# Performance work log

Measured on AMD Instinct MI355X. Metric: run time of the kernel, lower is better.

Reference implementation:

```python
import jax, jax.numpy as jnp
import numpy as np

B, W, C_BLK, N_EMBD, N_HEADS = 512, 128, 24, 32, 2


def setup_inputs() -> dict:
    key = jax.random.key(0)
    k1, k2, k3, k4 = jax.random.split(key, 4)
    x = jax.random.normal(k1, (B, W, C_BLK, N_EMBD), dtype=jnp.float32)
    x_end_idx = jax.random.randint(k2, (B, W), 0, C_BLK, dtype=jnp.int32)
    # nn.Linear(n_embd, 3*n_embd, bias=False): store transposed so y = x @ w
    w_attn = jax.random.normal(k3, (N_EMBD, 3 * N_EMBD), dtype=jnp.float32) * (1.0 / np.sqrt(N_EMBD))
    w_proj = jax.random.normal(k4, (N_EMBD, N_EMBD), dtype=jnp.float32) * (1.0 / np.sqrt(N_EMBD))
    return {"x": x, "x_end_idx": x_end_idx, "w_attn": w_attn, "w_proj": w_proj}


def reference(x, x_end_idx, w_attn, w_proj):
    # x: [B, W, c, C]; causal self-attention over the char axis c, per (batch, word).
    Bd, Wd, c, C = x.shape
    H = N_HEADS
    D = C // H
    qkv = x @ w_attn                               # [B, W, c, 3C]
    q, k, v = jnp.split(qkv, 3, axis=-1)
    # [B, W, H, c, D]
    q = q.reshape(Bd, Wd, c, H, D).transpose(0, 1, 3, 2, 4)
    k = k.reshape(Bd, Wd, c, H, D).transpose(0, 1, 3, 2, 4)
    v = v.reshape(Bd, Wd, c, H, D).transpose(0, 1, 3, 2, 4)
    scale = 1.0 / jnp.sqrt(jnp.asarray(D, dtype=x.dtype))
    scores = jnp.einsum('bwhqd,bwhkd->bwhqk', q, k) * scale   # [B, W, H, c, c]
    causal = jnp.tril(jnp.ones((c, c), dtype=bool))
    scores = jnp.where(causal, scores, jnp.asarray(-jnp.inf, dtype=scores.dtype))
    att = jax.nn.softmax(scores, axis=-1)
    out = jnp.einsum('bwhqk,bwhkd->bwhqd', att, v)            # [B, W, H, c, D]
    out = out.transpose(0, 1, 3, 2, 4).reshape(Bd, Wd, c, C)
    out = out @ w_proj                                        # c_proj (dropout in eval mode = identity)
    out = x + out                                             # residual
    # Vectorized last-token gather: pick out[b, w, x_end_idx[b, w], :]
    idx = x_end_idx[:, :, None, None].astype(jnp.int32)       # [B, W, 1, 1]
    samples = jnp.take_along_axis(out, jnp.broadcast_to(idx, (Bd, Wd, 1, C)), axis=2)
    return samples.squeeze(2)                                 # [B, W, C]
```

## Files before the change

### kernel.cpp

```cpp
#include <hip/hip_runtime.h>


#define CB      24
#define CC      32
#define DD      16
#define THREEC  96
#define NBW     (512 * 128)
#define WPB     4
#define XSS     34

struct __align__(16) WaveSmem {
    float xs[CB][XSS];
    float rks[2][CC];
    float es[CB][2];
    float ys[CC][2];
};

__device__ __forceinline__ void wave_fence() {
    __asm__ volatile("s_waitcnt lgkmcnt(0)" ::: "memory");
}

__global__ void prep_kernel(const float* __restrict__ w_attn,
                            const float* __restrict__ w_proj,
                            float* __restrict__ ws)
{
    const int t = blockIdx.x * 256 + threadIdx.x;
    if (t < 2048) {
        const int h = t >> 10, rem = t & 1023, cp = rem >> 5, c = rem & 31;
        float a = 0.f;
        #pragma unroll
        for (int d = 0; d < DD; ++d)
            a = fmaf(w_attn[cp * THREEC + 16 * h + d],
                     w_attn[c * THREEC + CC + 16 * h + d], a);
        ws[t] = a * 0.25f;
    } else {
        const int u = t - 2048;
        const int h = u >> 10, rem = u & 1023, c = rem >> 5, i = rem & 31;
        float a = 0.f;
        #pragma unroll
        for (int d = 0; d < DD; ++d)
            a = fmaf(w_attn[c * THREEC + 2 * CC + 16 * h + d],
                     w_proj[(16 * h + d) * CC + i], a);
        ws[t] = a;
    }
}

__global__ __launch_bounds__(256, 4) void char_attn_kernel(
    const float* __restrict__ x,
    const int*   __restrict__ xend,
    const float* __restrict__ ws,
    float*       __restrict__ out)
{
    __shared__ WaveSmem sm[WPB];

    const int tid  = threadIdx.x;
    const int lane = tid & 63;
    const int wave = tid >> 6;
    WaveSmem& S = sm[wave];

    const int i32  = lane & 31;
    const int half = lane >> 5;
    const int bid  = blockIdx.x * WPB + wave;

    const float* Mw = ws;
    const float* Nw = ws + 2048;

    float Mreg[CC];
    #pragma unroll
    for (int cp = 0; cp < CC; ++cp)
        Mreg[cp] = Mw[(half * CC + cp) * CC + i32];
    float Nreg[2][DD];
    #pragma unroll
    for (int h = 0; h < 2; ++h)
        #pragma unroll
        for (int k = 0; k < DD; ++k)
            Nreg[h][k] = Nw[(h * CC + half * DD + k) * CC + i32];

    const int qidx = xend[bid];
    const int L    = qidx + 1;
    const float* xb = x + (size_t)bid * (CB * CC);

    {
        const float2* xb2 = (const float2*)xb;
        const int n2 = L * (CC / 2);
        for (int t = lane; t < n2; t += 64) {
            float2 v = xb2[t];
            const int r = t >> 4, c = (t & 15) * 2;
            *(float2*)&S.xs[r][c] = v;
        }
    }
    wave_fence();

    {
        float a0 = 0.f, a1 = 0.f;
        #pragma unroll
        for (int cp = 0; cp < CC; cp += 2) {
            float2 xv = *(const float2*)&S.xs[qidx][cp];
            a0 = fmaf(xv.x, Mreg[cp],     a0);
            a1 = fmaf(xv.y, Mreg[cp + 1], a1);
        }
        S.rks[half][i32] = a0 + a1;
    }
    wave_fence();

    {
        float s0 = 0.f, s1 = 0.f;
        if (i32 <= qidx) {
            const int cb = half * DD;
            #pragma unroll
            for (int t = 0; t < DD; t += 2) {
                float2 xv = *(const float2*)&S.xs[i32][cb + t];
                s0 = fmaf(xv.x, S.rks[0][cb + t],     s0);
                s0 = fmaf(xv.y, S.rks[0][cb + t + 1], s0);
                s1 = fmaf(xv.x, S.rks[1][cb + t],     s1);
                s1 = fmaf(xv.y, S.rks[1][cb + t + 1], s1);
            }
        }
        s0 += __shfl_xor(s0, 32);
        s1 += __shfl_xor(s1, 32);
        const float e0 = (i32 <= qidx) ? __expf(s0) : 0.f;
        const float e1 = (i32 <= qidx) ? __expf(s1) : 0.f;
        if (half == 0 && i32 < CB)
            *(float2*)&S.es[i32][0] = make_float2(e0, e1);
    }
    wave_fence();

    {
        float y0 = 0.f, y1 = 0.f, ps0 = 0.f, ps1 = 0.f;
        #pragma unroll
        for (int jj = 0; jj < 12; ++jj) {
            const int j  = half * 12 + jj;
            const int jr = (j <= qidx) ? j : qidx;
            float2 ev = *(const float2*)&S.es[j][0];
            float  xv = S.xs[jr][i32];
            y0 = fmaf(ev.x, xv, y0);  ps0 += ev.x;
            y1 = fmaf(ev.y, xv, y1);  ps1 += ev.y;
        }
        y0  += __shfl_xor(y0, 32);
        y1  += __shfl_xor(y1, 32);
        ps0 += __shfl_xor(ps0, 32);
        ps1 += __shfl_xor(ps1, 32);
        if (half == 0)
            *(float2*)&S.ys[i32][0] = make_float2(y0 / ps0, y1 / ps1);
    }
    wave_fence();

    {
        float a0 = 0.f, a1 = 0.f;
        #pragma unroll
        for (int k = 0; k < DD; ++k) {
            const int c = half * DD + k;
            float2 yv = *(const float2*)&S.ys[c][0];
            a0 = fmaf(yv.x, Nreg[0][k], a0);
            a1 = fmaf(yv.y, Nreg[1][k], a1);
        }
        float a = a0 + a1;
        a += __shfl_xor(a, 32);
        if (half == 0)
            out[(size_t)bid * CC + i32] = a + S.xs[qidx][i32];
    }
}

extern "C" void kernel_launch(void* const* d_in, const int* in_sizes, int n_in,
                              void* d_out, int out_size, void* d_ws, size_t ws_size,
                              hipStream_t stream) {
    const float* x      = (const float*)d_in[0];
    const int*   xend   = (const int*)d_in[1];
    const float* w_attn = (const float*)d_in[2];
    const float* w_proj = (const float*)d_in[3];
    float* out = (float*)d_out;
    float* ws  = (float*)d_ws;

    prep_kernel<<<dim3(16), dim3(256), 0, stream>>>(w_attn, w_proj, ws);
    char_attn_kernel<<<dim3(NBW / WPB), dim3(WPB * 64), 0, stream>>>(
        x, xend, ws, out);
}
```

Baseline: 304.2 us.

## Process eight words per wave to amortize weight register loads

Each wave now loops over eight (batch, word) problems instead of one. The per-thread M and N weight registers are loaded once and reused across all eight, and the grid shrinks by the same factor. The shared-memory layouts change (row stride padded to 36, transposed rki and ys) so the inner products can use float4 LDS reads. The risk is less parallelism to hide global load latency, because the x loads inside the serial loop are not prefetched; grid size drops to 2048 blocks.

New measurement: 305.3 us. Within noise of the previous version (+0.4%).

```diff
diff --git a/kernel.cpp b/kernel.cpp
--- a/kernel.cpp
+++ b/kernel.cpp
@@ -7,13 +7,14 @@
 #define THREEC  96
 #define NBW     (512 * 128)
 #define WPB     4
-#define XSS     34
+#define PPW     8
+#define XSS     36
 
 struct __align__(16) WaveSmem {
     float xs[CB][XSS];
-    float rks[2][CC];
+    float rki[CC][2];
     float es[CB][2];
-    float ys[CC][2];
+    float ys[2][CC];
 };
 
 __device__ __forceinline__ void wave_fence() {
@@ -60,7 +61,8 @@
 
     const int i32  = lane & 31;
     const int half = lane >> 5;
-    const int bid  = blockIdx.x * WPB + wave;
+    const int wid  = blockIdx.x * WPB + wave;
+    const int pbase = wid * PPW;
 
     const float* Mw = ws;
     const float* Nw = ws + 2048;
@@ -76,88 +78,111 @@
         for (int k = 0; k < DD; ++k)
             Nreg[h][k] = Nw[(h * CC + half * DD + k) * CC + i32];
 
-    const int qidx = xend[bid];
-    const int L    = qidx + 1;
-    const float* xb = x + (size_t)bid * (CB * CC);
-
-    {
-        const float2* xb2 = (const float2*)xb;
-        const int n2 = L * (CC / 2);
-        for (int t = lane; t < n2; t += 64) {
-            float2 v = xb2[t];
-            const int r = t >> 4, c = (t & 15) * 2;
-            *(float2*)&S.xs[r][c] = v;
-        }
-    }
-    wave_fence();
-
-    {
-        float a0 = 0.f, a1 = 0.f;
-        #pragma unroll
-        for (int cp = 0; cp < CC; cp += 2) {
-            float2 xv = *(const float2*)&S.xs[qidx][cp];
-            a0 = fmaf(xv.x, Mreg[cp],     a0);
-            a1 = fmaf(xv.y, Mreg[cp + 1], a1);
-        }
-        S.rks[half][i32] = a0 + a1;
-    }
-    wave_fence();
-
-    {
-        float s0 = 0.f, s1 = 0.f;
-        if (i32 <= qidx) {
-            const int cb = half * DD;
+    #pragma unroll 1
+    for (int pi = 0; pi < PPW; ++pi) {
+        const int bid  = pbase + pi;
+        const int qidx = xend[bid];
+        const int L    = qidx + 1;
+        const float* xb = x + (size_t)bid * (CB * CC);
+
+        {
+            const float2* xb2 = (const float2*)xb;
+            const int n2 = L * (CC / 2);
+            for (int t = lane; t < n2; t += 64) {
+                float2 v = xb2[t];
+                const int r = t >> 4, c = (t & 15) * 2;
+                *(float2*)&S.xs[r][c] = v;
+            }
+        }
+        wave_fence();
+
+        {
+            const float4* xr = (const float4*)&S.xs[qidx][0];
+            float a0 = 0.f, a1 = 0.f;
             #pragma unroll
-            for (int t = 0; t < DD; t += 2) {
-                float2 xv = *(const float2*)&S.xs[i32][cb + t];
-                s0 = fmaf(xv.x, S.rks[0][cb + t],     s0);
-                s0 = fmaf(xv.y, S.rks[0][cb + t + 1], s0);
-                s1 = fmaf(xv.x, S.rks[1][cb + t],     s1);
-                s1 = fmaf(xv.y, S.rks[1][cb + t + 1], s1);
-            }
-        }
-        s0 += __shfl_xor(s0, 32);
-        s1 += __shfl_xor(s1, 32);
-        const float e0 = (i32 <= qidx) ? __expf(s0) : 0.f;
-        const float e1 = (i32 <= qidx) ? __expf(s1) : 0.f;
-        if (half == 0 && i32 < CB)
-            *(float2*)&S.es[i32][0] = make_float2(e0, e1);
-    }
-    wave_fence();
-
-    {
-        float y0 = 0.f, y1 = 0.f, ps0 = 0.f, ps1 = 0.f;
-        #pragma unroll
-        for (int jj = 0; jj < 12; ++jj) {
-            const int j  = half * 12 + jj;
-            const int jr = (j <= qidx) ? j : qidx;
-            float2 ev = *(const float2*)&S.es[j][0];
-            float  xv = S.xs[jr][i32];
-            y0 = fmaf(ev.x, xv, y0);  ps0 += ev.x;
-            y1 = fmaf(ev.y, xv, y1);  ps1 += ev.y;
-        }
-        y0  += __shfl_xor(y0, 32);
-        y1  += __shfl_xor(y1, 32);
-        ps0 += __shfl_xor(ps0, 32);
-        ps1 += __shfl_xor(ps1, 32);
-        if (half == 0)
-            *(float2*)&S.ys[i32][0] = make_float2(y0 / ps0, y1 / ps1);
-    }
-    wave_fence();
-
-    {
-        float a0 = 0.f, a1 = 0.f;
-        #pragma unroll
-        for (int k = 0; k < DD; ++k) {
-            const int c = half * DD + k;
-            float2 yv = *(const float2*)&S.ys[c][0];
-            a0 = fmaf(yv.x, Nreg[0][k], a0);
-            a1 = fmaf(yv.y, Nreg[1][k], a1);
-        }
-        float a = a0 + a1;
-        a += __shfl_xor(a, 32);
-        if (half == 0)
-            out[(size_t)bid * CC + i32] = a + S.xs[qidx][i32];
+            for (int t = 0; t < 8; ++t) {
+                float4 xv = xr[t];
+                a0 = fmaf(xv.x, Mreg[4 * t + 0], a0);
+                a1 = fmaf(xv.y, Mreg[4 * t + 1], a1);
+                a0 = fmaf(xv.z, Mreg[4 * t + 2], a0);
+                a1 = fmaf(xv.w, Mreg[4 * t + 3], a1);
+            }
+            S.rki[i32][half] = a0 + a1;
+        }
+        wave_fence();
+
+        {
+            float s0 = 0.f, s1 = 0.f;
+            if (i32 <= qidx) {
+                const int cb = half * DD;
+                const float4* xr = (const float4*)&S.xs[i32][cb];
+                const float4* rp = (const float4*)&S.rki[cb][0];
+                #pragma unroll
+                for (int t = 0; t < 4; ++t) {
+                    float4 xv = xr[t];
+                    float4 r01 = rp[2 * t];
+                    float4 r23 = rp[2 * t + 1];
+                    s0 = fmaf(xv.x, r01.x, s0);  s1 = fmaf(xv.x, r01.y, s1);
+                    s0 = fmaf(xv.y, r01.z, s0);  s1 = fmaf(xv.y, r01.w, s1);
+                    s0 = fmaf(xv.z, r23.x, s0);  s1 = fmaf(xv.z, r23.y, s1);
+                    s0 = fmaf(xv.w, r23.z, s0);  s1 = fmaf(xv.w, r23.w, s1);
+                }
+            }
+            s0 += __shfl_xor(s0, 32);
+            s1 += __shfl_xor(s1, 32);
+            const float e0 = (i32 <= qidx) ? __expf(s0) : 0.f;
+            const float e1 = (i32 <= qidx) ? __expf(s1) : 0.f;
+            if (half == 0 && i32 < CB)
+                *(float2*)&S.es[i32][0] = make_float2(e0, e1);
+        }
+        wave_fence();
+
+        {
+            float y0 = 0.f, y1 = 0.f, p0 = 0.f, p1 = 0.f;
+            #pragma unroll
+            for (int k = 0; k < 6; ++k) {
+                const int j0 = half * 12 + 2 * k;
+                float4 eq = *(const float4*)&S.es[j0][0];
+                const int r0 = (j0     <= qidx) ? j0     : qidx;
+                const int r1 = (j0 + 1 <= qidx) ? j0 + 1 : qidx;
+                float xv0 = S.xs[r0][i32];
+                float xv1 = S.xs[r1][i32];
+                y0 = fmaf(eq.x, xv0, y0);  y1 = fmaf(eq.y, xv0, y1);
+                p0 += eq.x;                p1 += eq.y;
+                y0 = fmaf(eq.z, xv1, y0);  y1 = fmaf(eq.w, xv1, y1);
+                p0 += eq.z;                p1 += eq.w;
+            }
+            y0 += __shfl_xor(y0, 32);
+            y1 += __shfl_xor(y1, 32);
+            p0 += __shfl_xor(p0, 32);
+            p1 += __shfl_xor(p1, 32);
+            if (half == 0) S.ys[0][i32] = y0 / p0;
+            else           S.ys[1][i32] = y1 / p1;
+        }
+        wave_fence();
+
+        {
+            const float4* y0p = (const float4*)&S.ys[0][half * DD];
+            const float4* y1p = (const float4*)&S.ys[1][half * DD];
+            float a0 = 0.f, a1 = 0.f;
+            #pragma unroll
+            for (int t = 0; t < 4; ++t) {
+                float4 u = y0p[t], w = y1p[t];
+                a0 = fmaf(u.x, Nreg[0][4 * t + 0], a0);
+                a1 = fmaf(w.x, Nreg[1][4 * t + 0], a1);
+                a0 = fmaf(u.y, Nreg[0][4 * t + 1], a0);
+                a1 = fmaf(w.y, Nreg[1][4 * t + 1], a1);
+                a0 = fmaf(u.z, Nreg[0][4 * t + 2], a0);
+                a1 = fmaf(w.z, Nreg[1][4 * t + 2], a1);
+                a0 = fmaf(u.w, Nreg[0][4 * t + 3], a0);
+                a1 = fmaf(w.w, Nreg[1][4 * t + 3], a1);
+            }
+            float a = a0 + a1;
+            a += __shfl_xor(a, 32);
+            if (half == 0)
+                out[(size_t)bid * CC + i32] = a + S.xs[qidx][i32];
+        }
+        wave_fence();
     }
 }
 
@@ -172,6 +197,6 @@
     float* ws  = (float*)d_ws;
 
     prep_kernel<<<dim3(16), dim3(256), 0, stream>>>(w_attn, w_proj, ws);
-    char_attn_kernel<<<dim3(NBW / WPB), dim3(WPB * 64), 0, stream>>>(
+    char_attn_kernel<<<dim3(NBW / (WPB * PPW)), dim3(WPB * 64), 0, stream>>>(
         x, xend, ws, out);
 }
```
